# Kernel optimization log

Hardware: AMD Instinct MI355X
Metric: run time of the kernel (lower is better)

## Reference

```python
import jax, jax.numpy as jnp
import numpy as np

N_NODES = 100000   # adj is [N, N], x is [N, D]
N_EDGES = 625000   # nnz of the COO adjacency
D_FEAT = 128       # embedding dim
EDGE_DROPOUT = 0.1


def setup_inputs() -> dict:
    key = jax.random.key(0)
    k1, k2, k3, k4 = jax.random.split(key, 4)
    x = jax.random.normal(k1, (N_NODES, D_FEAT), dtype=jnp.float32)
    edge_vals = jax.random.uniform(k2, (N_EDGES,), dtype=jnp.float32)
    edge_index = jax.random.randint(k3, (2, N_EDGES), 0, N_NODES)
    # training-mode edge dropout mask: keep edge iff u > edge_dropout
    keep_mask = jax.random.uniform(k4, (N_EDGES,)) > EDGE_DROPOUT
    return {"x": x, "edge_vals": edge_vals, "edge_index": edge_index, "keep_mask": keep_mask}


def reference(x, edge_vals, edge_index, keep_mask):
    # Dropping an edge from the COO tensor == zeroing its value in the SpMM.
    vals = jnp.where(keep_mask, edge_vals, jnp.zeros((), dtype=edge_vals.dtype))
    row = edge_index[0]  # destination rows of adj
    col = edge_index[1]  # source columns of adj
    # out[r] = sum_{e: row[e]==r} vals[e] * x[col[e]]   (torch.sparse.mm(adj, x))
    msgs = vals[:, None] * x[col]                      # [E, D]
    return jax.ops.segment_sum(msgs, row, num_segments=N_NODES)
```

## Files before the change

kernel.cpp:

```cpp
#include <hip/hip_runtime.h>

#define N_NODES 100000
#define N_EDGES 625000
#define D_FEAT  128

#define NBKT   98
#define CAPB   8192
#define EPB    2048
#define ABLOCKS ((N_EDGES + EPB - 1) / EPB)
#define CONV_BLOCKS (N_NODES * D_FEAT / 8 / 256)

#define BF_LO(u) __uint_as_float((u) << 16)
#define BF_HI(u) __uint_as_float((u) & 0xffff0000u)

__device__ __forceinline__ unsigned int rne_bf16(unsigned int u) {
    return (u + 0x7fffu + ((u >> 16) & 1u)) >> 16;
}

__global__ __launch_bounds__(256) void bucket_conv(
    const float* __restrict__ x, uint4* __restrict__ xb4,
    const int* __restrict__ ei, const int* __restrict__ keep,
    const float* __restrict__ vals, int* __restrict__ cursor,
    int2* __restrict__ pairs)
{
    int b = blockIdx.x;
    if (b < ABLOCKS) {
        __shared__ int hist[NBKT];
        __shared__ int run[NBKT];
        int t = threadIdx.x;
        for (int i = t; i < NBKT; i += 256) hist[i] = 0;
        __syncthreads();
        int base = b * EPB;
        int   r[8];
        bool  kp[8];
        #pragma unroll
        for (int j = 0; j < 8; ++j) {
            int e = base + j * 256 + t;
            bool k = false; int rr = 0;
            if (e < N_EDGES) { k = (keep[e] != 0); if (k) rr = ei[e]; }
            kp[j] = k; r[j] = rr;
            if (k) atomicAdd(&hist[rr >> 10], 1);
        }
        __syncthreads();
        for (int i = t; i < NBKT; i += 256) {
            int h = hist[i];
            run[i] = (h > 0) ? atomicAdd(&cursor[i], h) : 0;
        }
        __syncthreads();
        #pragma unroll
        for (int j = 0; j < 8; ++j) {
            if (!kp[j]) continue;
            int e  = base + j * 256 + t;
            int bk = r[j] >> 10;
            int pos = atomicAdd(&run[bk], 1);
            if (pos < CAPB) {
                int rl = r[j] & 1023;
                int2 pr = { ei[N_EDGES + e] | (rl << 17), __float_as_int(vals[e]) };
                pairs[(long long)bk * CAPB + pos] = pr;
            }
        }
    } else {
        int i = (b - ABLOCKS) * 256 + threadIdx.x;
        const float4* x4 = reinterpret_cast<const float4*>(x);
        float4 v0 = x4[i * 2], v1 = x4[i * 2 + 1];
        unsigned int a  = rne_bf16(__float_as_uint(v0.x));
        unsigned int bq = rne_bf16(__float_as_uint(v0.y));
        unsigned int c  = rne_bf16(__float_as_uint(v0.z));
        unsigned int d  = rne_bf16(__float_as_uint(v0.w));
        unsigned int e2 = rne_bf16(__float_as_uint(v1.x));
        unsigned int f  = rne_bf16(__float_as_uint(v1.y));
        unsigned int g2 = rne_bf16(__float_as_uint(v1.z));
        unsigned int h  = rne_bf16(__float_as_uint(v1.w));
        uint4 o = { a | (bq << 16), c | (d << 16), e2 | (f << 16), g2 | (h << 16) };
        xb4[i] = o;
    }
}

__global__ __launch_bounds__(256) void build_csr(
    const int* __restrict__ cursor, const int2* __restrict__ pairs,
    int2* __restrict__ fin, int2* __restrict__ rowinfo)
{
    __shared__ int hist[1024];
    __shared__ int ssum[256];
    int b = blockIdx.x;
    int t = threadIdx.x;
    int t4 = t * 4;
    #pragma unroll
    for (int i = 0; i < 4; ++i) hist[t4 + i] = 0;
    __syncthreads();
    int n = cursor[b]; if (n > CAPB) n = CAPB;
    const int2* reg = pairs + (long long)b * CAPB;
    for (int i = t; i < n; i += 256)
        atomicAdd(&hist[reg[i].x >> 17], 1);
    __syncthreads();
    int c0 = hist[t4], c1 = hist[t4 + 1], c2 = hist[t4 + 2], c3 = hist[t4 + 3];
    ssum[t] = c0 + c1 + c2 + c3;
    __syncthreads();
    for (int off = 1; off < 256; off <<= 1) {
        int add = (t >= off) ? ssum[t - off] : 0;
        __syncthreads();
        ssum[t] += add;
        __syncthreads();
    }
    int excl = (t == 0) ? 0 : ssum[t - 1];
    hist[t4]     = excl;
    hist[t4 + 1] = excl + c0;
    hist[t4 + 2] = excl + c0 + c1;
    hist[t4 + 3] = excl + c0 + c1 + c2;
    int rbase = b << 10;
    int gbase = b * CAPB;
    int cc[4] = { c0, c1, c2, c3 };
    #pragma unroll
    for (int i = 0; i < 4; ++i) {
        int row = rbase + t4 + i;
        if (row < N_NODES) {
            int2 ri = { gbase + hist[t4 + i], cc[i] };
            rowinfo[row] = ri;
        }
    }
    __syncthreads();
    for (int i = t; i < n; i += 256) {
        int2 pr = reg[i];
        int rl = pr.x >> 17;
        int pos = atomicAdd(&hist[rl], 1);
        int2 o = { pr.x & 0x1FFFF, pr.y };
        fin[gbase + pos] = o;
    }
}

__global__ __launch_bounds__(256) void gather_csr_bf16(
    const uint4* __restrict__ xb4, const int2* __restrict__ rowinfo,
    const int2* __restrict__ fin, float4* __restrict__ out4)
{
    int gid = blockIdx.x * blockDim.x + threadIdx.x;
    int wave = gid >> 6;
    int lane = threadIdx.x & 63;
    int sub = lane >> 4, l16 = lane & 15;
    int row = wave * 4 + sub;
    if (row >= N_NODES) return;
    int2 ri = rowinfo[row];
    const int2* bp = fin + ri.x;
    int n = ri.y;

    float a0=0,a1=0,a2=0,a3=0,a4=0,a5=0,a6=0,a7=0;
    float c0=0,c1=0,c2=0,c3=0,c4=0,c5=0,c6=0,c7=0;
    int p = 0;
    for (; p + 2 <= n; p += 2) {
        int2 e0 = bp[p], e1 = bp[p + 1];
        uint4 g0 = xb4[(long long)e0.x * 16 + l16];
        uint4 g1 = xb4[(long long)e1.x * 16 + l16];
        float v0 = __int_as_float(e0.y), v1 = __int_as_float(e1.y);
        a0 += v0 * BF_LO(g0.x); a1 += v0 * BF_HI(g0.x);
        a2 += v0 * BF_LO(g0.y); a3 += v0 * BF_HI(g0.y);
        a4 += v0 * BF_LO(g0.z); a5 += v0 * BF_HI(g0.z);
        a6 += v0 * BF_LO(g0.w); a7 += v0 * BF_HI(g0.w);
        c0 += v1 * BF_LO(g1.x); c1 += v1 * BF_HI(g1.x);
        c2 += v1 * BF_LO(g1.y); c3 += v1 * BF_HI(g1.y);
        c4 += v1 * BF_LO(g1.z); c5 += v1 * BF_HI(g1.z);
        c6 += v1 * BF_LO(g1.w); c7 += v1 * BF_HI(g1.w);
    }
    if (p < n) {
        int2 e = bp[p];
        uint4 g = xb4[(long long)e.x * 16 + l16];
        float v = __int_as_float(e.y);
        a0 += v * BF_LO(g.x); a1 += v * BF_HI(g.x);
        a2 += v * BF_LO(g.y); a3 += v * BF_HI(g.y);
        a4 += v * BF_LO(g.z); a5 += v * BF_HI(g.z);
        a6 += v * BF_LO(g.w); a7 += v * BF_HI(g.w);
    }
    float4 o0 = { a0 + c0, a1 + c1, a2 + c2, a3 + c3 };
    float4 o1 = { a4 + c4, a5 + c5, a6 + c6, a7 + c7 };
    long long ob = (long long)row * 32 + l16 * 2;
    out4[ob]     = o0;
    out4[ob + 1] = o1;
}

__global__ __launch_bounds__(256) void gather_csr_f32(
    const float* __restrict__ x, const int2* __restrict__ rowinfo,
    const int2* __restrict__ fin, float* __restrict__ out)
{
    int gid = blockIdx.x * blockDim.x + threadIdx.x;
    int row = gid >> 6;
    if (row >= N_NODES) return;
    int lane = threadIdx.x & 63;
    int2 ri = rowinfo[row];
    const int2* bp = fin + ri.x;
    int n = ri.y;
    int d = lane * 2;
    float a0 = 0.f, b0 = 0.f, a1 = 0.f, b1 = 0.f;
    int p = 0;
    for (; p + 2 <= n; p += 2) {
        int2 e0 = bp[p], e1 = bp[p + 1];
        float2 x0 = *reinterpret_cast<const float2*>(x + (long long)e0.x * D_FEAT + d);
        float2 x1 = *reinterpret_cast<const float2*>(x + (long long)e1.x * D_FEAT + d);
        float v0 = __int_as_float(e0.y), v1 = __int_as_float(e1.y);
        a0 += v0 * x0.x; b0 += v0 * x0.y;
        a1 += v1 * x1.x; b1 += v1 * x1.y;
    }
    if (p < n) {
        int2 e = bp[p];
        float2 xv = *reinterpret_cast<const float2*>(x + (long long)e.x * D_FEAT + d);
        float v = __int_as_float(e.y);
        a0 += v * xv.x; b0 += v * xv.y;
    }
    float2 o = { a0 + a1, b0 + b1 };
    *reinterpret_cast<float2*>(out + (long long)row * D_FEAT + d) = o;
}

static inline size_t alignup(size_t v) { return (v + 511) / 512 * 512; }

extern "C" void kernel_launch(void* const* d_in, const int* in_sizes, int n_in,
                              void* d_out, int out_size, void* d_ws, size_t ws_size,
                              hipStream_t stream) {
    const float* x    = (const float*)d_in[0];
    const float* vals = (const float*)d_in[1];
    const int*   ei   = (const int*)d_in[2];
    const int*   keep = (const int*)d_in[3];
    float* out = (float*)d_out;

    const size_t sz_xb   = alignup((size_t)N_NODES * D_FEAT * 2);
    const size_t sz_cur  = 512;
    const size_t sz_pair = (size_t)NBKT * CAPB * 8;
    const size_t sz_fin  = (size_t)NBKT * CAPB * 8;
    const size_t sz_ri   = alignup((size_t)N_NODES * 8);
    const bool use_bf16 = ws_size >= sz_xb + sz_cur + sz_pair + sz_fin + sz_ri;

    char* ws = (char*)d_ws;
    uint4* xb4 = nullptr;
    if (use_bf16) { xb4 = (uint4*)ws; ws += sz_xb; }
    int*  cursor  = (int*)ws;   ws += sz_cur;
    int2* pairs   = (int2*)ws;  ws += sz_pair;
    int2* fin     = (int2*)ws;  ws += sz_fin;
    int2* rowinfo = (int2*)ws;

    hipMemsetAsync(cursor, 0, NBKT * sizeof(int), stream);

    if (use_bf16) {
        bucket_conv<<<ABLOCKS + CONV_BLOCKS, 256, 0, stream>>>(
            x, xb4, ei, keep, vals, cursor, pairs);
    } else {
        bucket_conv<<<ABLOCKS, 256, 0, stream>>>(
            x, xb4, ei, keep, vals, cursor, pairs);
    }
    build_csr<<<NBKT, 256, 0, stream>>>(cursor, pairs, fin, rowinfo);

    if (use_bf16) {
        const long long gthreads = (long long)((N_NODES + 3) / 4) * 64;
        gather_csr_bf16<<<(int)((gthreads + 255) / 256), 256, 0, stream>>>(
            xb4, rowinfo, fin, (float4*)out);
    } else {
        const long long gthreads = (long long)N_NODES * 64;
        gather_csr_f32<<<(int)((gthreads + 255) / 256), 256, 0, stream>>>(
            x, rowinfo, fin, out);
    }
}
```

Baseline: 80.96 us.

## Replace global bucket cursors with per-block chunked bucketing and shared-memory CSR build

Each scatter block now writes kept edges into its own fixed-size chunk per row bucket, using only shared-memory atomics. Per-block counts go to a table, which removes the global atomic cursor and the memset launch. build_csr prefix-sums the chunk counts, gathers the bucket's edges into LDS, and then does the row histogram and scatter from shared memory. In exchange, chunk capacity is capped at 48 edges per block per bucket, so overflowing edges would be silently dropped. The per-chunk copy loop is serial per thread and uses 64KB+ of LDS per block.

```diff
diff --git a/kernel.cpp b/kernel.cpp
--- a/kernel.cpp
+++ b/kernel.cpp
@@ -4,10 +4,13 @@
 #define N_EDGES 625000
 #define D_FEAT  128
 
-#define NBKT   98
-#define CAPB   8192
-#define EPB    2048
-#define ABLOCKS ((N_EDGES + EPB - 1) / EPB)
+#define BKT_SHIFT 10
+#define BKT_ROWS  1024
+#define NBKT      ((N_NODES + BKT_ROWS - 1) / BKT_ROWS)
+#define EPB       2048
+#define ABLOCKS   ((N_EDGES + EPB - 1) / EPB)
+#define CHCAP     48
+#define CAPB      8192
 #define CONV_BLOCKS (N_NODES * D_FEAT / 8 / 256)
 
 #define BF_LO(u) __uint_as_float((u) << 16)
@@ -20,81 +23,64 @@
 __global__ __launch_bounds__(256) void bucket_conv(
     const float* __restrict__ x, uint4* __restrict__ xb4,
     const int* __restrict__ ei, const int* __restrict__ keep,
-    const float* __restrict__ vals, int* __restrict__ cursor,
-    int2* __restrict__ pairs)
+    const float* __restrict__ vals,
+    int*  __restrict__ counts,
+    int2* __restrict__ chunks)
 {
     int b = blockIdx.x;
     if (b < ABLOCKS) {
-        __shared__ int hist[NBKT];
-        __shared__ int run[NBKT];
+        __shared__ int cur[NBKT];
         int t = threadIdx.x;
-        for (int i = t; i < NBKT; i += 256) hist[i] = 0;
+        if (t < NBKT) cur[t] = 0;
         __syncthreads();
         int base = b * EPB;
-        int   r[8];
-        bool  kp[8];
         #pragma unroll
         for (int j = 0; j < 8; ++j) {
             int e = base + j * 256 + t;
-            bool k = false; int rr = 0;
-            if (e < N_EDGES) { k = (keep[e] != 0); if (k) rr = ei[e]; }
-            kp[j] = k; r[j] = rr;
-            if (k) atomicAdd(&hist[rr >> 10], 1);
-        }
-        __syncthreads();
-        for (int i = t; i < NBKT; i += 256) {
-            int h = hist[i];
-            run[i] = (h > 0) ? atomicAdd(&cursor[i], h) : 0;
-        }
-        __syncthreads();
-        #pragma unroll
-        for (int j = 0; j < 8; ++j) {
-            if (!kp[j]) continue;
-            int e  = base + j * 256 + t;
-            int bk = r[j] >> 10;
-            int pos = atomicAdd(&run[bk], 1);
-            if (pos < CAPB) {
-                int rl = r[j] & 1023;
-                int2 pr = { ei[N_EDGES + e] | (rl << 17), __float_as_int(vals[e]) };
-                pairs[(long long)bk * CAPB + pos] = pr;
+            if (e < N_EDGES && keep[e]) {
+                int r = ei[e];
+                int bk = r >> BKT_SHIFT;
+                int pos = atomicAdd(&cur[bk], 1);
+                if (pos < CHCAP) {
+                    int2 pr = { ei[N_EDGES + e] | ((r & (BKT_ROWS - 1)) << 17),
+                                __float_as_int(vals[e]) };
+                    chunks[((long long)b * NBKT + bk) * CHCAP + pos] = pr;
+                }
             }
         }
+        __syncthreads();
+        if (t < NBKT) counts[b * NBKT + t] = min(cur[t], CHCAP);
     } else {
         int i = (b - ABLOCKS) * 256 + threadIdx.x;
         const float4* x4 = reinterpret_cast<const float4*>(x);
         float4 v0 = x4[i * 2], v1 = x4[i * 2 + 1];
         unsigned int a  = rne_bf16(__float_as_uint(v0.x));
-        unsigned int bq = rne_bf16(__float_as_uint(v0.y));
+        unsigned int bb = rne_bf16(__float_as_uint(v0.y));
         unsigned int c  = rne_bf16(__float_as_uint(v0.z));
         unsigned int d  = rne_bf16(__float_as_uint(v0.w));
         unsigned int e2 = rne_bf16(__float_as_uint(v1.x));
         unsigned int f  = rne_bf16(__float_as_uint(v1.y));
-        unsigned int g2 = rne_bf16(__float_as_uint(v1.z));
+        unsigned int g  = rne_bf16(__float_as_uint(v1.z));
         unsigned int h  = rne_bf16(__float_as_uint(v1.w));
-        uint4 o = { a | (bq << 16), c | (d << 16), e2 | (f << 16), g2 | (h << 16) };
+        uint4 o = { a | (bb << 16), c | (d << 16), e2 | (f << 16), g | (h << 16) };
         xb4[i] = o;
     }
 }
 
 __global__ __launch_bounds__(256) void build_csr(
-    const int* __restrict__ cursor, const int2* __restrict__ pairs,
+    const int* __restrict__ counts, const int2* __restrict__ chunks,
     int2* __restrict__ fin, int2* __restrict__ rowinfo)
 {
-    __shared__ int hist[1024];
-    __shared__ int ssum[256];
-    int b = blockIdx.x;
-    int t = threadIdx.x;
-    int t4 = t * 4;
-    #pragma unroll
-    for (int i = 0; i < 4; ++i) hist[t4 + i] = 0;
-    __syncthreads();
-    int n = cursor[b]; if (n > CAPB) n = CAPB;
-    const int2* reg = pairs + (long long)b * CAPB;
-    for (int i = t; i < n; i += 256)
-        atomicAdd(&hist[reg[i].x >> 17], 1);
-    __syncthreads();
-    int c0 = hist[t4], c1 = hist[t4 + 1], c2 = hist[t4 + 2], c3 = hist[t4 + 3];
-    ssum[t] = c0 + c1 + c2 + c3;
+    __shared__ int2 ebuf[CAPB];
+    __shared__ int  cbase[ABLOCKS + 1];
+    __shared__ int  hist[BKT_ROWS];
+    __shared__ int  ssum[256];
+    int b = blockIdx.x, t = threadIdx.x;
+
+    int i0 = 2 * t, i1 = 2 * t + 1;
+    int c0 = (i0 < ABLOCKS) ? counts[i0 * NBKT + b] : 0;
+    int c1 = (i1 < ABLOCKS) ? counts[i1 * NBKT + b] : 0;
+    ssum[t] = c0 + c1;
     __syncthreads();
     for (int off = 1; off < 256; off <<= 1) {
         int add = (t >= off) ? ssum[t - off] : 0;
@@ -103,28 +89,64 @@
         __syncthreads();
     }
     int excl = (t == 0) ? 0 : ssum[t - 1];
-    hist[t4]     = excl;
-    hist[t4 + 1] = excl + c0;
-    hist[t4 + 2] = excl + c0 + c1;
-    hist[t4 + 3] = excl + c0 + c1 + c2;
-    int rbase = b << 10;
+    if (i0 < ABLOCKS) cbase[i0] = excl;
+    if (i1 < ABLOCKS) cbase[i1] = excl + c0;
+    if (t == 255) cbase[ABLOCKS] = ssum[255];
+    __syncthreads();
+    int ntot = cbase[ABLOCKS]; if (ntot > CAPB) ntot = CAPB;
+
+    for (int c = t; c < ABLOCKS; c += 256) {
+        int n = counts[c * NBKT + b];
+        int cb = cbase[c];
+        const int2* src = chunks + ((long long)c * NBKT + b) * CHCAP;
+        for (int k = 0; k < n; ++k) {
+            int dst = cb + k;
+            if (dst < CAPB) ebuf[dst] = src[k];
+        }
+    }
+    for (int i = t; i < BKT_ROWS; i += 256) hist[i] = 0;
+    __syncthreads();
+
+    for (int i = t; i < ntot; i += 256)
+        atomicAdd(&hist[(ebuf[i].x >> 17) & (BKT_ROWS - 1)], 1);
+    __syncthreads();
+
+    int t4 = t * 4;
+    int h0 = hist[t4], h1 = hist[t4 + 1], h2 = hist[t4 + 2], h3 = hist[t4 + 3];
+    ssum[t] = h0 + h1 + h2 + h3;
+    __syncthreads();
+    for (int off = 1; off < 256; off <<= 1) {
+        int add = (t >= off) ? ssum[t - off] : 0;
+        __syncthreads();
+        ssum[t] += add;
+        __syncthreads();
+    }
+    int ex = (t == 0) ? 0 : ssum[t - 1];
+    int s0 = ex, s1 = ex + h0, s2 = ex + h0 + h1, s3 = ex + h0 + h1 + h2;
+    hist[t4] = s0; hist[t4 + 1] = s1; hist[t4 + 2] = s2; hist[t4 + 3] = s3;
+
+    int rbase = b << BKT_SHIFT;
     int gbase = b * CAPB;
-    int cc[4] = { c0, c1, c2, c3 };
+    int st[4] = { s0, s1, s2, s3 };
+    int hh[4] = { h0, h1, h2, h3 };
     #pragma unroll
     for (int i = 0; i < 4; ++i) {
         int row = rbase + t4 + i;
         if (row < N_NODES) {
-            int2 ri = { gbase + hist[t4 + i], cc[i] };
+            int2 ri = { gbase + st[i], hh[i] };
             rowinfo[row] = ri;
         }
     }
     __syncthreads();
-    for (int i = t; i < n; i += 256) {
-        int2 pr = reg[i];
-        int rl = pr.x >> 17;
+
+    for (int i = t; i < ntot; i += 256) {
+        int2 pr = ebuf[i];
+        int rl = (pr.x >> 17) & (BKT_ROWS - 1);
         int pos = atomicAdd(&hist[rl], 1);
-        int2 o = { pr.x & 0x1FFFF, pr.y };
-        fin[gbase + pos] = o;
+        if (pos < CAPB) {
+            int2 o = { pr.x & 0x1FFFF, pr.y };
+            fin[gbase + pos] = o;
+        }
     }
 }
 
@@ -218,31 +240,26 @@
     const int*   keep = (const int*)d_in[3];
     float* out = (float*)d_out;
 
-    const size_t sz_xb   = alignup((size_t)N_NODES * D_FEAT * 2);
-    const size_t sz_cur  = 512;
-    const size_t sz_pair = (size_t)NBKT * CAPB * 8;
-    const size_t sz_fin  = (size_t)NBKT * CAPB * 8;
-    const size_t sz_ri   = alignup((size_t)N_NODES * 8);
-    const bool use_bf16 = ws_size >= sz_xb + sz_cur + sz_pair + sz_fin + sz_ri;
+    const size_t sz_xb     = alignup((size_t)N_NODES * D_FEAT * 2);
+    const size_t sz_counts = alignup((size_t)ABLOCKS * NBKT * 4);
+    const size_t sz_chunks = alignup((size_t)ABLOCKS * NBKT * CHCAP * 8);
+    const size_t sz_fin    = alignup((size_t)NBKT * CAPB * 8);
+    const size_t sz_ri     = alignup((size_t)N_NODES * 8);
+    const bool use_bf16 =
+        ws_size >= sz_xb + sz_counts + sz_chunks + sz_fin + sz_ri;
 
     char* ws = (char*)d_ws;
     uint4* xb4 = nullptr;
     if (use_bf16) { xb4 = (uint4*)ws; ws += sz_xb; }
-    int*  cursor  = (int*)ws;   ws += sz_cur;
-    int2* pairs   = (int2*)ws;  ws += sz_pair;
+    int*  counts  = (int*)ws;   ws += sz_counts;
+    int2* chunks  = (int2*)ws;  ws += sz_chunks;
     int2* fin     = (int2*)ws;  ws += sz_fin;
     int2* rowinfo = (int2*)ws;
 
-    hipMemsetAsync(cursor, 0, NBKT * sizeof(int), stream);
-
-    if (use_bf16) {
-        bucket_conv<<<ABLOCKS + CONV_BLOCKS, 256, 0, stream>>>(
-            x, xb4, ei, keep, vals, cursor, pairs);
-    } else {
-        bucket_conv<<<ABLOCKS, 256, 0, stream>>>(
-            x, xb4, ei, keep, vals, cursor, pairs);
-    }
-    build_csr<<<NBKT, 256, 0, stream>>>(cursor, pairs, fin, rowinfo);
+    const int ablocks_total = use_bf16 ? (ABLOCKS + CONV_BLOCKS) : ABLOCKS;
+    bucket_conv<<<ablocks_total, 256, 0, stream>>>(
+        x, xb4, ei, keep, vals, counts, chunks);
+    build_csr<<<NBKT, 256, 0, stream>>>(counts, chunks, fin, rowinfo);
 
     if (use_bf16) {
         const long long gthreads = (long long)((N_NODES + 3) / 4) * 64;
```

After: 72.93 us. 1.11x faster.
